# Performance work log

Measured on AMD Instinct MI355X. Metric: run time of the kernel, lower is better.

## Reference

```python
import jax, jax.numpy as jnp
import numpy as np

N = 100000
IN_DIM, HID_DIM, OUT_DIM = 256, 128, 128
DROPOUT_P = 0.1


def _gcn_conv(x, src, dst, W, b, n_nodes):
    # PyG GCNConv: x' = D^{-1/2} (A+I) D^{-1/2} (x W^T) + b
    # src/dst already include self-loops.
    h = x @ W.T  # (N, out)
    deg = jax.ops.segment_sum(jnp.ones_like(dst, dtype=h.dtype), dst,
                              num_segments=n_nodes)
    dinv = jnp.where(deg > 0, jax.lax.rsqrt(deg), 0.0)
    norm = dinv[src] * dinv[dst]                # (E+N,)
    msg = h[src] * norm[:, None]                # (E+N, out) - dominant traffic
    out = jax.ops.segment_sum(msg, dst, num_segments=n_nodes)
    return out + b


def setup_inputs() -> dict:
    key = jax.random.key(0)
    k1, k2, k3, k4, k5, k6 = jax.random.split(key, 6)
    X = jax.random.normal(k1, (N, IN_DIM), dtype=jnp.float32)
    edge_index = jax.random.randint(k2, (2, 1600000), 0, N, dtype=jnp.int64)
    # Glorot-ish init for linear weights (stored torch-style: (out, in))
    W1 = jax.random.normal(k3, (HID_DIM, IN_DIM), dtype=jnp.float32) / np.sqrt(IN_DIM)
    b1 = jnp.zeros((HID_DIM,), dtype=jnp.float32)
    W2 = jax.random.normal(k4, (OUT_DIM, HID_DIM), dtype=jnp.float32) / np.sqrt(HID_DIM)
    b2 = jnp.zeros((OUT_DIM,), dtype=jnp.float32)
    return {"X": X, "edge_index": edge_index, "W1": W1, "b1": b1,
            "W2": W2, "b2": b2}


def reference(X, edge_index, W1, b1, W2, b2):
    n = X.shape[0]
    loops = jnp.arange(n, dtype=edge_index.dtype)
    src = jnp.concatenate([edge_index[0], loops])
    dst = jnp.concatenate([edge_index[1], loops])

    h = _gcn_conv(X, src, dst, W1, b1, n)
    h = jax.nn.relu(h)
    # training-mode dropout with a fixed key (deterministic baseline)
    keep = jax.random.bernoulli(jax.random.key(42), 1.0 - DROPOUT_P, h.shape)
    h = jnp.where(keep, h / (1.0 - DROPOUT_P), 0.0)
    h = _gcn_conv(h, src, dst, W2, b2, n)
    return h
```

## Files before the change

kernel.cpp:

```cpp
#include <hip/hip_runtime.h>
#include <stdint.h>

#define IN_DIM 256
#define HID 128
#define BKT_BITS 6
#define BKT_SZ 64
#define MAXBKT 2048
#define NB_BLK 256

typedef __attribute__((ext_vector_type(8))) short short8v;
typedef __attribute__((ext_vector_type(4))) float f32x4;

__device__ __forceinline__ unsigned short f2bf(float f) {
    unsigned u = __float_as_uint(f);
    unsigned rnd = 0x7FFFu + ((u >> 16) & 1u);
    return (unsigned short)((u + rnd) >> 16);
}
__device__ __forceinline__ float bflo(unsigned v) { return __uint_as_float(v << 16); }
__device__ __forceinline__ float bfhi(unsigned v) { return __uint_as_float(v & 0xFFFF0000u); }

__device__ __forceinline__ unsigned rotl32(unsigned x, int r) {
    return (x << r) | (x >> (32 - r));
}
__device__ __forceinline__ float dropout_scale(unsigned idx) {
    const unsigned ks0 = 0u, ks1 = 42u, ks2 = 0x1BD11BF0u;
    unsigned x0 = 0u + ks0;
    unsigned x1 = idx + ks1;
#define TF_ROUND(r) { x0 += x1; x1 = rotl32(x1, r); x1 ^= x0; }
    TF_ROUND(13) TF_ROUND(15) TF_ROUND(26) TF_ROUND(6)
    x0 += ks1; x1 += ks2 + 1u;
    TF_ROUND(17) TF_ROUND(29) TF_ROUND(16) TF_ROUND(24)
    x0 += ks2; x1 += ks0 + 2u;
    TF_ROUND(13) TF_ROUND(15) TF_ROUND(26) TF_ROUND(6)
    x0 += ks0; x1 += ks1 + 3u;
    TF_ROUND(17) TF_ROUND(29) TF_ROUND(16) TF_ROUND(24)
    x0 += ks1; x1 += ks2 + 4u;
    TF_ROUND(13) TF_ROUND(15) TF_ROUND(26) TF_ROUND(6)
    x0 += ks2; x1 += ks0 + 5u;
#undef TF_ROUND
    unsigned bits = x0 ^ x1;
    float u = __uint_as_float(0x3F800000u | (bits >> 9)) - 1.0f;
    return (u < 0.9f) ? (1.0f / 0.9f) : 0.0f;
}

__global__ __launch_bounds__(256) void part_count(const int* __restrict__ dst,
                                                  int* __restrict__ counts,
                                                  int E, int nbkt, int per) {
    __shared__ int lh[MAXBKT];
    for (int i = threadIdx.x; i < nbkt; i += 256) lh[i] = 0;
    __syncthreads();
    int blk = blockIdx.x;
    int beg = blk * per, end = min(E, beg + per);
    for (int i = beg + threadIdx.x; i < end; i += 256)
        atomicAdd(&lh[dst[i] >> BKT_BITS], 1);
    __syncthreads();
    for (int b = threadIdx.x; b < nbkt; b += 256)
        counts[b * NB_BLK + blk] = lh[b];
}

__global__ __launch_bounds__(256) void scan2_local(const int* __restrict__ in,
                                                   int* __restrict__ out,
                                                   int* __restrict__ bsum, int M) {
    __shared__ int lds[256];
    int t = threadIdx.x;
    int base = blockIdx.x * 2048 + t * 8;
    int x[8], v[8];
    if (base + 7 < M) {
        int4 a = *(const int4*)(in + base);
        int4 b = *(const int4*)(in + base + 4);
        x[0] = a.x; x[1] = a.y; x[2] = a.z; x[3] = a.w;
        x[4] = b.x; x[5] = b.y; x[6] = b.z; x[7] = b.w;
    } else {
        for (int j = 0; j < 8; ++j) x[j] = (base + j < M) ? in[base + j] : 0;
    }
    int s = 0;
    for (int j = 0; j < 8; ++j) { v[j] = s; s += x[j]; }
    lds[t] = s;
    __syncthreads();
    for (int d = 1; d < 256; d <<= 1) {
        int val = lds[t];
        int add = (t >= d) ? lds[t - d] : 0;
        __syncthreads();
        lds[t] = val + add;
        __syncthreads();
    }
    int excl = lds[t] - s;
    for (int j = 0; j < 8; ++j)
        if (base + j < M) out[base + j] = excl + v[j];
    if (t == 255) bsum[blockIdx.x] = lds[255];
}
__global__ __launch_bounds__(256) void scan2_bsums(int* __restrict__ bsum, int nb) {
    __shared__ int lds[256];
    int t = threadIdx.x;
    int orig = (t < nb) ? bsum[t] : 0;
    lds[t] = orig;
    __syncthreads();
    for (int d = 1; d < 256; d <<= 1) {
        int val = lds[t];
        int add = (t >= d) ? lds[t - d] : 0;
        __syncthreads();
        lds[t] = val + add;
        __syncthreads();
    }
    if (t < nb) bsum[t] = lds[t] - orig;
}
__global__ void scan2_add(int* __restrict__ out, const int* __restrict__ bsum, int M) {
    int i = blockIdx.x * blockDim.x + threadIdx.x;
    if (i < M) out[i] += bsum[i >> 11];
}

__global__ __launch_bounds__(256) void part_scatter(const int* __restrict__ src,
                                                    const int* __restrict__ dst,
                                                    const int* __restrict__ cbase,
                                                    unsigned* __restrict__ packed,
                                                    int E, int nbkt, int per) {
    __shared__ int cur[MAXBKT];
    int blk = blockIdx.x;
    for (int b = threadIdx.x; b < nbkt; b += 256)
        cur[b] = cbase[b * NB_BLK + blk];
    __syncthreads();
    int beg = blk * per, end = min(E, beg + per);
    for (int i = beg + threadIdx.x; i < end; i += 256) {
        int d = dst[i];
        int pos = atomicAdd(&cur[d >> BKT_BITS], 1);
        packed[pos] = ((unsigned)src[i] << BKT_BITS) | (unsigned)(d & (BKT_SZ - 1));
    }
}

__global__ void extract_bbase(const int* __restrict__ cbase, int* __restrict__ bbase,
                              int nbkt, int E) {
    int b = blockIdx.x * blockDim.x + threadIdx.x;
    if (b < nbkt) bbase[b] = cbase[b * NB_BLK];
    if (b == nbkt) bbase[nbkt] = E;
}

__global__ __launch_bounds__(256) void bucket_finalize(const unsigned* __restrict__ packed,
                                                       const int* __restrict__ bbase,
                                                       int* __restrict__ ssrc,
                                                       int* __restrict__ offs,
                                                       float* __restrict__ dinv, int N) {
    __shared__ int hist[BKT_SZ];
    __shared__ int cur[BKT_SZ];
    int b = blockIdx.x;
    int t = threadIdx.x;
    int beg = bbase[b], end = bbase[b + 1];
    if (t < BKT_SZ) hist[t] = 0;
    __syncthreads();
    for (int i = beg + t; i < end; i += 256)
        atomicAdd(&hist[packed[i] & (BKT_SZ - 1)], 1);
    __syncthreads();
    if (t < BKT_SZ) cur[t] = hist[t];
    __syncthreads();
    for (int d = 1; d < BKT_SZ; d <<= 1) {
        int val = 0;
        if (t < BKT_SZ) { val = cur[t]; if (t >= d) val += cur[t - d]; }
        __syncthreads();
        if (t < BKT_SZ) cur[t] = val;
        __syncthreads();
    }
    if (t < BKT_SZ) {
        int node = b * BKT_SZ + t;
        int excl = cur[t] - hist[t];
        if (node < N) {
            offs[node] = beg + excl;
            dinv[node] = rsqrtf((float)(hist[t] + 1));
        }
        cur[t] = excl;
    }
    __syncthreads();
    for (int i = beg + t; i < end; i += 256) {
        unsigned p = packed[i];
        int dl = (int)(p & (BKT_SZ - 1));
        int pos = atomicAdd(&cur[dl], 1);
        ssrc[beg + pos] = (int)(p >> BKT_BITS);
    }
}

__global__ void cvt_w(const float* __restrict__ W, unsigned short* __restrict__ Wb, int n) {
    int i = blockIdx.x * blockDim.x + threadIdx.x;
    if (i < n) Wb[i] = f2bf(W[i]);
}

#define WP 264
#define AP 40
template <int A_BF16>
__global__ __launch_bounds__(256) void gemm_mfma(const void* __restrict__ Ap,
                                                 const unsigned short* __restrict__ Wb,
                                                 const float* __restrict__ scale,
                                                 unsigned short* __restrict__ C,
                                                 int M, int K) {
    __shared__ unsigned short Wlds[128 * WP];
    __shared__ unsigned short Alds[64 * AP];
    const int t = threadIdx.x;
    const int bm = blockIdx.x * 64;

    const int kc = K >> 3;
    for (int c = t; c < 128 * kc; c += 256) {
        int row = c / kc, ko = c % kc;
        short8v w = *(const short8v*)(Wb + (size_t)row * K + ko * 8);
        *(short8v*)(&Wlds[row * WP + ko * 8]) = w;
    }

    const int w = t >> 6, l = t & 63;
    const int lr = l & 15, lk = l >> 4;
    const int sr = t >> 2, sc = t & 3;

    f32x4 acc[8] = {};

    for (int kb = 0; kb < K; kb += 32) {
        if (A_BF16) {
            short8v v = {};
            if (bm + sr < M)
                v = *(const short8v*)((const unsigned short*)Ap + (size_t)(bm + sr) * K + kb + sc * 8);
            *(short8v*)(&Alds[sr * AP + sc * 8]) = v;
        } else {
            short8v u = {};
            if (bm + sr < M) {
                const float* arow = (const float*)Ap + (size_t)(bm + sr) * K + kb + sc * 8;
                float4 f0 = *(const float4*)(arow);
                float4 f1 = *(const float4*)(arow + 4);
                u[0] = (short)f2bf(f0.x); u[1] = (short)f2bf(f0.y);
                u[2] = (short)f2bf(f0.z); u[3] = (short)f2bf(f0.w);
                u[4] = (short)f2bf(f1.x); u[5] = (short)f2bf(f1.y);
                u[6] = (short)f2bf(f1.z); u[7] = (short)f2bf(f1.w);
            }
            *(short8v*)(&Alds[sr * AP + sc * 8]) = u;
        }
        __syncthreads();

        short8v a = *(const short8v*)(&Alds[(w * 16 + lr) * AP + lk * 8]);
#pragma unroll
        for (int cb = 0; cb < 8; ++cb) {
            short8v b = *(const short8v*)(&Wlds[(cb * 16 + lr) * WP + kb + lk * 8]);
            acc[cb] = __builtin_amdgcn_mfma_f32_16x16x32_bf16(a, b, acc[cb], 0, 0, 0);
        }
        __syncthreads();
    }

    float scv[4];
#pragma unroll
    for (int j = 0; j < 4; ++j) {
        int row = bm + w * 16 + lk * 4 + j;
        scv[j] = (row < M) ? scale[row] : 0.f;
    }
#pragma unroll
    for (int cb = 0; cb < 8; ++cb) {
#pragma unroll
        for (int j = 0; j < 4; ++j) {
            int row = bm + w * 16 + lk * 4 + j;
            int col = cb * 16 + lr;
            if (row < M) C[(size_t)row * 128 + col] = f2bf(acc[cb][j] * scv[j]);
        }
    }
}

template <int MODE>
__global__ __launch_bounds__(256) void aggregate_csr(const unsigned* __restrict__ h,
                                                     const int* __restrict__ soff,
                                                     const int* __restrict__ ssrc,
                                                     const float* __restrict__ dinv,
                                                     const float* __restrict__ bias,
                                                     void* __restrict__ outp,
                                                     int N, int E) {
    int n = blockIdx.x * 4 + (threadIdx.x >> 6);
    if (n >= N) return;
    const int lane = threadIdx.x & 63;
    const int g = lane >> 4;
    const int f0 = lane & 15;
    int start = soff[n];
    int end = (n + 1 < N) ? soff[n + 1] : E;
    float dn = dinv[n];

    float a0 = 0.f, a1 = 0.f, a2 = 0.f, a3 = 0.f,
          a4 = 0.f, a5 = 0.f, a6 = 0.f, a7 = 0.f;

    for (int i = start; i < end; i += 8) {
        int i0 = i + g, i1 = i + g + 4;
        int s0 = (i0 < end) ? ssrc[i0] : N;
        int s1 = (i1 < end) ? ssrc[i1] : N;
        uint4 v0 = *(const uint4*)(h + (size_t)s0 * 64 + f0 * 4);
        uint4 v1 = *(const uint4*)(h + (size_t)s1 * 64 + f0 * 4);
        a0 += bflo(v0.x); a1 += bfhi(v0.x);
        a2 += bflo(v0.y); a3 += bfhi(v0.y);
        a4 += bflo(v0.z); a5 += bfhi(v0.z);
        a6 += bflo(v0.w); a7 += bfhi(v0.w);
        a0 += bflo(v1.x); a1 += bfhi(v1.x);
        a2 += bflo(v1.y); a3 += bfhi(v1.y);
        a4 += bflo(v1.z); a5 += bfhi(v1.z);
        a6 += bflo(v1.w); a7 += bfhi(v1.w);
    }

    a0 += __shfl_xor(a0, 16, 64); a0 += __shfl_xor(a0, 32, 64);
    a1 += __shfl_xor(a1, 16, 64); a1 += __shfl_xor(a1, 32, 64);
    a2 += __shfl_xor(a2, 16, 64); a2 += __shfl_xor(a2, 32, 64);
    a3 += __shfl_xor(a3, 16, 64); a3 += __shfl_xor(a3, 32, 64);
    a4 += __shfl_xor(a4, 16, 64); a4 += __shfl_xor(a4, 32, 64);
    a5 += __shfl_xor(a5, 16, 64); a5 += __shfl_xor(a5, 32, 64);
    a6 += __shfl_xor(a6, 16, 64); a6 += __shfl_xor(a6, 32, 64);
    a7 += __shfl_xor(a7, 16, 64); a7 += __shfl_xor(a7, 32, 64);

    uint4 hv = *(const uint4*)(h + (size_t)n * 64 + f0 * 4);
    unsigned hvg = (g == 0) ? hv.x : (g == 1) ? hv.y : (g == 2) ? hv.z : hv.w;
    float sx, sy;
    if (g == 0)      { sx = a0; sy = a1; }
    else if (g == 1) { sx = a2; sy = a3; }
    else if (g == 2) { sx = a4; sy = a5; }
    else             { sx = a6; sy = a7; }

    float ax = (sx + bflo(hvg)) * dn;
    float ay = (sy + bfhi(hvg)) * dn;
    float2 bv = ((const float2*)bias)[f0 * 4 + g];
    ax += bv.x;
    ay += bv.y;
    int fi = f0 * 8 + g * 2;
    if (MODE == 1) {
        unsigned idx = (unsigned)n * 128u + (unsigned)fi;
        ax = fmaxf(ax, 0.f) * dropout_scale(idx);
        ay = fmaxf(ay, 0.f) * dropout_scale(idx + 1u);
        ((unsigned*)outp)[(size_t)n * 64 + f0 * 4 + g] =
            (unsigned)f2bf(ax) | ((unsigned)f2bf(ay) << 16);
    } else {
        ((float2*)outp)[(size_t)n * 64 + f0 * 4 + g] = make_float2(ax, ay);
    }
}

extern "C" void kernel_launch(void* const* d_in, const int* in_sizes, int n_in,
                              void* d_out, int out_size, void* d_ws, size_t ws_size,
                              hipStream_t stream) {
    const float* X  = (const float*)d_in[0];
    const int*   ei = (const int*)d_in[1];
    const float* W1 = (const float*)d_in[2];
    const float* b1 = (const float*)d_in[3];
    const float* W2 = (const float*)d_in[4];
    const float* b2 = (const float*)d_in[5];
    float* out = (float*)d_out;

    const int N = in_sizes[0] / IN_DIM;
    const int E = in_sizes[1] / 2;
    const int* src = ei;
    const int* dst = ei + E;
    const int total = N * HID;
    const size_t N4 = (size_t)N * 4;
    const size_t tot2 = (size_t)total * 2;
    const int NBKT = (N + BKT_SZ - 1) >> BKT_BITS;
    const int M = NBKT * NB_BLK;
    const int per = (E + NB_BLK - 1) / NB_BLK;
    const int snb = (M + 2047) / 2048;

    char* ws = (char*)d_ws;
    size_t off = 0;
    unsigned short* hA = (unsigned short*)(ws + off); off += tot2 + HID * 2;
    unsigned short* hB = (unsigned short*)(ws + off); off += tot2;
    float* dinv = (float*)(ws + off); off += N4;
    int* offs   = (int*)(ws + off); off += N4;
    int* counts = (int*)(ws + off); off += (size_t)M * 4;
    int* cbase  = (int*)(ws + off); off += (size_t)M * 4;
    int* bsum   = (int*)(ws + off); off += 4096;
    int* bbase  = (int*)(ws + off); off += (size_t)(MAXBKT + 1) * 4;
    unsigned* packed = (unsigned*)(ws + off); off += (size_t)E * 4;
    int* ssrc   = (int*)(ws + off); off += (size_t)E * 4;
    unsigned short* Wb1 = (unsigned short*)(ws + off); off += (size_t)HID * IN_DIM * 2;
    unsigned short* Wb2 = (unsigned short*)(ws + off);

    hipMemsetAsync(hA + (size_t)N * HID, 0, HID * 2, stream);

    cvt_w<<<(HID * IN_DIM + 255) / 256, 256, 0, stream>>>(W1, Wb1, HID * IN_DIM);
    cvt_w<<<(HID * HID + 255) / 256, 256, 0, stream>>>(W2, Wb2, HID * HID);
    part_count<<<NB_BLK, 256, 0, stream>>>(dst, counts, E, NBKT, per);
    scan2_local<<<snb, 256, 0, stream>>>(counts, cbase, bsum, M);
    scan2_bsums<<<1, 256, 0, stream>>>(bsum, snb);
    scan2_add<<<(M + 255) / 256, 256, 0, stream>>>(cbase, bsum, M);
    part_scatter<<<NB_BLK, 256, 0, stream>>>(src, dst, cbase, packed, E, NBKT, per);
    extract_bbase<<<(NBKT + 256) / 256, 256, 0, stream>>>(cbase, bbase, NBKT, E);
    bucket_finalize<<<NBKT, 256, 0, stream>>>(packed, bbase, ssrc, offs, dinv, N);

    gemm_mfma<0><<<(N + 63) / 64, 256, 0, stream>>>(X, Wb1, dinv, hA, N, IN_DIM);
    aggregate_csr<1><<<(N + 3) / 4, 256, 0, stream>>>((const unsigned*)hA, offs, ssrc,
                                                      dinv, b1, hB, N, E);
    gemm_mfma<1><<<(N + 63) / 64, 256, 0, stream>>>(hB, Wb2, dinv, hA, N, HID);
    aggregate_csr<2><<<(N + 3) / 4, 256, 0, stream>>>((const unsigned*)hA, offs, ssrc,
                                                      dinv, b2, out, N, E);
}
```

Measured before the change: 307.3 us.

## Keep W fragments in registers and stage full A tile in LDS for MFMA GEMM

```diff
diff --git a/kernel.cpp b/kernel.cpp
--- a/kernel.cpp
+++ b/kernel.cpp
@@ -181,75 +181,90 @@
     if (i < n) Wb[i] = f2bf(W[i]);
 }
 
-#define WP 264
-#define AP 40
-template <int A_BF16>
+template <int K, int A_BF16>
 __global__ __launch_bounds__(256) void gemm_mfma(const void* __restrict__ Ap,
                                                  const unsigned short* __restrict__ Wb,
                                                  const float* __restrict__ scale,
                                                  unsigned short* __restrict__ C,
-                                                 int M, int K) {
-    __shared__ unsigned short Wlds[128 * WP];
-    __shared__ unsigned short Alds[64 * AP];
+                                                 int M) {
+    constexpr int NKB = K / 32;
+    constexpr int APAD = K + 8;
+    __shared__ unsigned short Alds[64 * APAD];
     const int t = threadIdx.x;
     const int bm = blockIdx.x * 64;
-
-    const int kc = K >> 3;
-    for (int c = t; c < 128 * kc; c += 256) {
-        int row = c / kc, ko = c % kc;
-        short8v w = *(const short8v*)(Wb + (size_t)row * K + ko * 8);
-        *(short8v*)(&Wlds[row * WP + ko * 8]) = w;
-    }
-
     const int w = t >> 6, l = t & 63;
     const int lr = l & 15, lk = l >> 4;
-    const int sr = t >> 2, sc = t & 3;
-
-    f32x4 acc[8] = {};
-
-    for (int kb = 0; kb < K; kb += 32) {
-        if (A_BF16) {
+
+    short8v bfrag[2][NKB];
+#pragma unroll
+    for (int cbi = 0; cbi < 2; ++cbi) {
+        int col = (w * 2 + cbi) * 16 + lr;
+#pragma unroll
+        for (int kb = 0; kb < NKB; ++kb)
+            bfrag[cbi][kb] = *(const short8v*)(Wb + (size_t)col * K + kb * 32 + lk * 8);
+    }
+
+    if constexpr (A_BF16) {
+        constexpr int STEPS = 64 * K / (256 * 8);
+        const unsigned short* Abase = (const unsigned short*)Ap;
+#pragma unroll
+        for (int i = 0; i < STEPS; ++i) {
+            int flat = (i * 256 + t) * 8;
+            int row = flat / K;
+            int o = flat % K;
             short8v v = {};
-            if (bm + sr < M)
-                v = *(const short8v*)((const unsigned short*)Ap + (size_t)(bm + sr) * K + kb + sc * 8);
-            *(short8v*)(&Alds[sr * AP + sc * 8]) = v;
-        } else {
+            if (bm + row < M)
+                v = *(const short8v*)(Abase + (size_t)(bm + row) * K + o);
+            *(short8v*)(&Alds[row * APAD + o]) = v;
+        }
+    } else {
+        constexpr int STEPS = 64 * K / (256 * 8);
+        const float* Abase = (const float*)Ap;
+#pragma unroll
+        for (int i = 0; i < STEPS; ++i) {
+            int flat = (i * 256 + t) * 8;
+            int row = flat / K;
+            int o = flat % K;
             short8v u = {};
-            if (bm + sr < M) {
-                const float* arow = (const float*)Ap + (size_t)(bm + sr) * K + kb + sc * 8;
-                float4 f0 = *(const float4*)(arow);
-                float4 f1 = *(const float4*)(arow + 4);
+            if (bm + row < M) {
+                const float* p = Abase + (size_t)(bm + row) * K + o;
+                float4 f0 = *(const float4*)(p);
+                float4 f1 = *(const float4*)(p + 4);
                 u[0] = (short)f2bf(f0.x); u[1] = (short)f2bf(f0.y);
                 u[2] = (short)f2bf(f0.z); u[3] = (short)f2bf(f0.w);
                 u[4] = (short)f2bf(f1.x); u[5] = (short)f2bf(f1.y);
                 u[6] = (short)f2bf(f1.z); u[7] = (short)f2bf(f1.w);
             }
-            *(short8v*)(&Alds[sr * AP + sc * 8]) = u;
-        }
-        __syncthreads();
-
-        short8v a = *(const short8v*)(&Alds[(w * 16 + lr) * AP + lk * 8]);
-#pragma unroll
-        for (int cb = 0; cb < 8; ++cb) {
-            short8v b = *(const short8v*)(&Wlds[(cb * 16 + lr) * WP + kb + lk * 8]);
-            acc[cb] = __builtin_amdgcn_mfma_f32_16x16x32_bf16(a, b, acc[cb], 0, 0, 0);
-        }
-        __syncthreads();
-    }
-
-    float scv[4];
-#pragma unroll
-    for (int j = 0; j < 4; ++j) {
-        int row = bm + w * 16 + lk * 4 + j;
-        scv[j] = (row < M) ? scale[row] : 0.f;
-    }
-#pragma unroll
-    for (int cb = 0; cb < 8; ++cb) {
-#pragma unroll
-        for (int j = 0; j < 4; ++j) {
-            int row = bm + w * 16 + lk * 4 + j;
-            int col = cb * 16 + lr;
-            if (row < M) C[(size_t)row * 128 + col] = f2bf(acc[cb][j] * scv[j]);
+            *(short8v*)(&Alds[row * APAD + o]) = u;
+        }
+    }
+    __syncthreads();
+
+#pragma unroll
+    for (int m = 0; m < 4; ++m) {
+        short8v afr[NKB];
+#pragma unroll
+        for (int kb = 0; kb < NKB; ++kb)
+            afr[kb] = *(const short8v*)(&Alds[(m * 16 + lr) * APAD + kb * 32 + lk * 8]);
+        f32x4 acc[2] = {};
+#pragma unroll
+        for (int kb = 0; kb < NKB; ++kb) {
+            acc[0] = __builtin_amdgcn_mfma_f32_16x16x32_bf16(afr[kb], bfrag[0][kb], acc[0], 0, 0, 0);
+            acc[1] = __builtin_amdgcn_mfma_f32_16x16x32_bf16(afr[kb], bfrag[1][kb], acc[1], 0, 0, 0);
+        }
+        int r0 = bm + m * 16 + lk * 4;
+        float scv[4];
+#pragma unroll
+        for (int j = 0; j < 4; ++j)
+            scv[j] = (r0 + j < M) ? scale[r0 + j] : 0.f;
+#pragma unroll
+        for (int cbi = 0; cbi < 2; ++cbi) {
+            int col = (w * 2 + cbi) * 16 + lr;
+#pragma unroll
+            for (int j = 0; j < 4; ++j) {
+                if (r0 + j < M)
+                    C[(size_t)(r0 + j) * 128 + col] = f2bf(acc[cbi][j] * scv[j]);
+            }
         }
     }
 }
@@ -374,10 +389,10 @@
     extract_bbase<<<(NBKT + 256) / 256, 256, 0, stream>>>(cbase, bbase, NBKT, E);
     bucket_finalize<<<NBKT, 256, 0, stream>>>(packed, bbase, ssrc, offs, dinv, N);
 
-    gemm_mfma<0><<<(N + 63) / 64, 256, 0, stream>>>(X, Wb1, dinv, hA, N, IN_DIM);
+    gemm_mfma<256, 0><<<(N + 63) / 64, 256, 0, stream>>>(X, Wb1, dinv, hA, N);
     aggregate_csr<1><<<(N + 3) / 4, 256, 0, stream>>>((const unsigned*)hA, offs, ssrc,
                                                       dinv, b1, hB, N, E);
-    gemm_mfma<1><<<(N + 63) / 64, 256, 0, stream>>>(hB, Wb2, dinv, hA, N, HID);
+    gemm_mfma<128, 1><<<(N + 63) / 64, 256, 0, stream>>>(hB, Wb2, dinv, hA, N);
     aggregate_csr<2><<<(N + 3) / 4, 256, 0, stream>>>((const unsigned*)hA, offs, ssrc,
                                                       dinv, b2, out, N, E);
 }
```

Result: faster. 263.8 us (-14.2%).
